# Optimization experiments

Hardware: AMD Instinct MI355X
Metric: run time of the kernel (lower is better)

## Reference

```python
import jax, jax.numpy as jnp
import numpy as np

NUM_SCOPES, NUM_DECOMPS, BATCH, NUM_IN, NUM_SUMS = 32, 8, 256, 256, 256


def setup_inputs() -> dict:
    key = jax.random.key(0)
    k1, k2 = jax.random.split(key)
    # x: log-probabilities from children, shape [scopes, decomps, batch, num_nodes_in]
    x = jax.random.normal(k1, (NUM_SCOPES, NUM_DECOMPS, BATCH, NUM_IN), dtype=jnp.float32)
    # accumulators: positive weights, shape [scopes, decomps, num_nodes_in, num_sums]
    accumulators = jax.random.uniform(
        k2, (NUM_SCOPES, NUM_DECOMPS, NUM_IN, NUM_SUMS), dtype=jnp.float32,
        minval=1e-3, maxval=1.0)
    return {"x": x, "accumulators": accumulators}


def _logmatmul(x, logw):
    # out[s,d,b,j] = logsumexp_i( x[s,d,b,i] + logw[s,d,i,j] )
    # Stable form: factor out per-row / per-col maxes, do a real GEMM in linear space.
    xmax = jnp.max(x, axis=3, keepdims=True)            # [s,d,b,1]
    wmax = jnp.max(logw, axis=2, keepdims=True)         # [s,d,1,j]
    y = jnp.einsum('sdbi,sdij->sdbj', jnp.exp(x - xmax), jnp.exp(logw - wmax))
    return jnp.log(y) + xmax + wmax                     # [s,d,b,j]


def reference(x, accumulators):
    # Default path: logspace_accumulators=False, backprop_mode=GRADIENT
    log_weights = jax.nn.log_softmax(jnp.log(accumulators), axis=2)
    return _logmatmul(x, log_weights)
```

## Files before the change

kernel.cpp:

```cpp
#include <hip/hip_runtime.h>


#define NB  256
#define NI  256
#define NJ  256
#define BH  128

typedef __attribute__((ext_vector_type(8))) short bf16x8;
typedef __attribute__((ext_vector_type(4))) float f32x4;

__device__ __forceinline__ unsigned short f2bf(float f) {
  unsigned int u = __float_as_uint(f);
  u += 0x7FFFu + ((u >> 16) & 1u);
  return (unsigned short)(u >> 16);
}

__global__ __launch_bounds__(512, 2)
void densesum_kernel(const float* __restrict__ x,
                     const float* __restrict__ acc,
                     float* __restrict__ out) {
  const int sd = blockIdx.x;
  const float* xb = x   + (size_t)sd * NB * NI;
  const float* ab = acc + (size_t)sd * NI * NJ;
  float*       ob = out + (size_t)sd * NB * NJ;

  __shared__ unsigned short As[BH * 64];
  __shared__ unsigned short Bs[NJ * NI];
  __shared__ float colpart[8 * NJ];
  __shared__ float logS[NJ];

  const int tid  = threadIdx.x;
  const int lane = tid & 63;
  const int wid  = tid >> 6;
  const int wr   = wid >> 2;
  const int wc   = wid & 3;
  const int l15  = lane & 15;
  const int lk   = lane >> 4;
  const int r    = (lane >> 1) & 3;
  const bool s1 = (r & 1), s2 = (r & 2);

  f32x4 C[4][4];
  float bsum0 = 0.f, bsum1 = 0.f, bsum2 = 0.f, bsum3 = 0.f;
  float4 pa[4];
  float4 pb[8];

  auto zeroC = [&]() {
    #pragma unroll
    for (int m = 0; m < 4; ++m)
      #pragma unroll
      for (int n = 0; n < 4; ++n)
        C[m][n] = (f32x4){0.f, 0.f, 0.f, 0.f};
  };

  auto loadA = [&](const float* xh, int kc) {
    #pragma unroll
    for (int it = 0; it < 4; ++it) {
      int q  = tid + it * 512;
      int b  = q >> 4;
      int c0 = (q & 15) * 4;
      pa[it] = *reinterpret_cast<const float4*>(xh + (size_t)b * NI + kc * 64 + c0);
    }
  };
  auto loadB = [&](int kc) {
    #pragma unroll
    for (int t = 0; t < 2; ++t) {
      int q  = tid + t * 512;
      int kl = (q >> 6) * 4;
      int jb = (q & 63) * 4;
      const float* src = ab + (size_t)(kc * 64 + kl) * NJ + jb;
      pb[t * 4 + 0] = *reinterpret_cast<const float4*>(src);
      pb[t * 4 + 1] = *reinterpret_cast<const float4*>(src + NJ);
      pb[t * 4 + 2] = *reinterpret_cast<const float4*>(src + 2 * NJ);
      pb[t * 4 + 3] = *reinterpret_cast<const float4*>(src + 3 * NJ);
    }
  };
  auto convA = [&]() {
    #pragma unroll
    for (int it = 0; it < 4; ++it) {
      int q  = tid + it * 512;
      int b  = q >> 4;
      int c0 = (q & 15) * 4;
      ushort4 h;
      h.x = f2bf(__expf(pa[it].x));
      h.y = f2bf(__expf(pa[it].y));
      h.z = f2bf(__expf(pa[it].z));
      h.w = f2bf(__expf(pa[it].w));
      *reinterpret_cast<ushort4*>(&As[b * 64 + (c0 ^ ((b & 7) << 3))]) = h;
    }
  };
  auto convB = [&](int kc) {
    #pragma unroll
    for (int t = 0; t < 2; ++t) {
      int q   = tid + t * 512;
      int kl  = (q >> 6) * 4;
      int jb  = (q & 63) * 4;
      int kg  = kc * 64 + kl;
      float4 v0 = pb[t * 4 + 0], v1 = pb[t * 4 + 1];
      float4 v2 = pb[t * 4 + 2], v3 = pb[t * 4 + 3];
      #define ROT(v, u0, u1, u2, u3)                                            \
        { float t0 = s1 ? v.y : v.x, t1 = s1 ? v.z : v.y,                       \
                t2 = s1 ? v.w : v.z, t3 = s1 ? v.x : v.w;                       \
          u0 = s2 ? t2 : t0; u1 = s2 ? t3 : t1;                                 \
          u2 = s2 ? t0 : t2; u3 = s2 ? t1 : t3; }
      float a00, a01, a02, a03; ROT(v0, a00, a01, a02, a03);
      float a10, a11, a12, a13; ROT(v1, a10, a11, a12, a13);
      float a20, a21, a22, a23; ROT(v2, a20, a21, a22, a23);
      float a30, a31, a32, a33; ROT(v3, a30, a31, a32, a33);
      #undef ROT
      #define STORE_COL(cc, w0, w1, w2, w3)                                     \
        { int jc = jb + ((cc + r) & 3);                                         \
          bsum##cc += w0 + w1 + w2 + w3;                                        \
          ushort4 h; h.x = f2bf(w0); h.y = f2bf(w1);                            \
          h.z = f2bf(w2); h.w = f2bf(w3);                                       \
          *reinterpret_cast<ushort4*>(&Bs[jc * NI + (kg ^ ((jc & 7) << 3))]) = h; }
      STORE_COL(0, a00, a10, a20, a30);
      STORE_COL(1, a01, a11, a21, a31);
      STORE_COL(2, a02, a12, a22, a32);
      STORE_COL(3, a03, a13, a23, a33);
      #undef STORE_COL
    }
  };
  auto mfmaChunk = [&](int kc) {
    #pragma unroll
    for (int ks = 0; ks < 2; ++ks) {
      const int ka = ks * 32 + 8 * lk;
      const int kg = kc * 64 + ka;
      bf16x8 bfr[4];
      #pragma unroll
      for (int n = 0; n < 4; ++n) {
        int row = wc * 64 + n * 16 + l15;
        bfr[n] = *reinterpret_cast<const bf16x8*>(&Bs[row * NI + (kg ^ ((row & 7) << 3))]);
      }
      #pragma unroll
      for (int m = 0; m < 4; ++m) {
        int row = wr * 64 + m * 16 + l15;
        bf16x8 af = *reinterpret_cast<const bf16x8*>(&As[row * 64 + (ka ^ ((row & 7) << 3))]);
        #pragma unroll
        for (int n = 0; n < 4; ++n)
          C[m][n] = __builtin_amdgcn_mfma_f32_16x16x32_bf16(af, bfr[n], C[m][n], 0, 0, 0);
      }
    }
  };
  auto epilogue = [&](int bh) {
    float* obh = ob + (size_t)bh * BH * NJ;
    #pragma unroll
    for (int m = 0; m < 4; ++m) {
      int b0 = wr * 64 + m * 16 + lk * 4;
      #pragma unroll
      for (int n = 0; n < 4; ++n) {
        int j = wc * 64 + n * 16 + l15;
        float ls = logS[j];
        #pragma unroll
        for (int rr = 0; rr < 4; ++rr) {
          obh[(size_t)(b0 + rr) * NJ + j] = __logf(C[m][n][rr]) - ls;
        }
      }
    }
  };

  loadA(xb, 0);
  loadB(0);
  zeroC();
  for (int kc = 0; kc < 4; ++kc) {
    convA();
    convB(kc);
    __syncthreads();
    if (kc < 3) {
      loadA(xb, kc + 1);
      loadB(kc + 1);
    } else {
      loadA(xb + (size_t)BH * NI, 0);
    }
    mfmaChunk(kc);
    __syncthreads();
  }

  {
    int jb = lane * 4;
    colpart[wid * NJ + jb + ((0 + r) & 3)] = bsum0;
    colpart[wid * NJ + jb + ((1 + r) & 3)] = bsum1;
    colpart[wid * NJ + jb + ((2 + r) & 3)] = bsum2;
    colpart[wid * NJ + jb + ((3 + r) & 3)] = bsum3;
  }
  __syncthreads();
  if (tid < NJ) {
    float s = 0.f;
    #pragma unroll
    for (int c = 0; c < 8; ++c) s += colpart[c * NJ + tid];
    logS[tid] = __logf(s);
  }
  __syncthreads();

  epilogue(0);

  zeroC();
  for (int kc = 0; kc < 4; ++kc) {
    convA();
    __syncthreads();
    if (kc < 3) loadA(xb + (size_t)BH * NI, kc + 1);
    mfmaChunk(kc);
    __syncthreads();
  }

  epilogue(1);
}

extern "C" void kernel_launch(void* const* d_in, const int* in_sizes, int n_in,
                              void* d_out, int out_size, void* d_ws, size_t ws_size,
                              hipStream_t stream) {
  const float* x   = (const float*)d_in[0];
  const float* acc = (const float*)d_in[1];
  float* out = (float*)d_out;
  hipLaunchKernelGGL(densesum_kernel, dim3(256), dim3(512), 0, stream, x, acc, out);
}
```

Baseline: 38.25 us.

## Double block size to 1024 threads with 16 waves splitting output columns

Launches 1024 threads per block instead of 512 and rearranges the wave grid to 2x8, so each wave computes a 64x32 output tile instead of 64x64. The load and convert work per thread for A and B is halved, and the column-sum reduction gains an extra pairwise stage through shared memory. The aim is more waves per CU to hide memory latency and exp/convert cost. In exchange the register budget per thread is tighter, each B fragment is reused over fewer columns, and the extra reduction stage adds a barrier.

```diff
diff --git a/kernel.cpp b/kernel.cpp
--- a/kernel.cpp
+++ b/kernel.cpp
@@ -15,7 +15,7 @@
   return (unsigned short)(u >> 16);
 }
 
-__global__ __launch_bounds__(512, 2)
+__global__ __launch_bounds__(1024, 4)
 void densesum_kernel(const float* __restrict__ x,
                      const float* __restrict__ acc,
                      float* __restrict__ out) {
@@ -26,58 +26,54 @@
 
   __shared__ unsigned short As[BH * 64];
   __shared__ unsigned short Bs[NJ * NI];
-  __shared__ float colpart[8 * NJ];
+  __shared__ float redbuf[8 * NJ];
   __shared__ float logS[NJ];
 
   const int tid  = threadIdx.x;
   const int lane = tid & 63;
   const int wid  = tid >> 6;
-  const int wr   = wid >> 2;
-  const int wc   = wid & 3;
+  const int wr   = wid >> 3;
+  const int wc   = wid & 7;
   const int l15  = lane & 15;
   const int lk   = lane >> 4;
   const int r    = (lane >> 1) & 3;
   const bool s1 = (r & 1), s2 = (r & 2);
-
-  f32x4 C[4][4];
+  const int kp   = wid;
+  const int jbB  = lane * 4;
+
+  f32x4 C[4][2];
   float bsum0 = 0.f, bsum1 = 0.f, bsum2 = 0.f, bsum3 = 0.f;
-  float4 pa[4];
-  float4 pb[8];
+  float4 pa[2];
+  float4 pb[4];
 
   auto zeroC = [&]() {
     #pragma unroll
     for (int m = 0; m < 4; ++m)
       #pragma unroll
-      for (int n = 0; n < 4; ++n)
+      for (int n = 0; n < 2; ++n)
         C[m][n] = (f32x4){0.f, 0.f, 0.f, 0.f};
   };
 
   auto loadA = [&](const float* xh, int kc) {
     #pragma unroll
-    for (int it = 0; it < 4; ++it) {
-      int q  = tid + it * 512;
+    for (int it = 0; it < 2; ++it) {
+      int q  = tid + it * 1024;
       int b  = q >> 4;
       int c0 = (q & 15) * 4;
       pa[it] = *reinterpret_cast<const float4*>(xh + (size_t)b * NI + kc * 64 + c0);
     }
   };
   auto loadB = [&](int kc) {
-    #pragma unroll
-    for (int t = 0; t < 2; ++t) {
-      int q  = tid + t * 512;
-      int kl = (q >> 6) * 4;
-      int jb = (q & 63) * 4;
-      const float* src = ab + (size_t)(kc * 64 + kl) * NJ + jb;
-      pb[t * 4 + 0] = *reinterpret_cast<const float4*>(src);
-      pb[t * 4 + 1] = *reinterpret_cast<const float4*>(src + NJ);
-      pb[t * 4 + 2] = *reinterpret_cast<const float4*>(src + 2 * NJ);
-      pb[t * 4 + 3] = *reinterpret_cast<const float4*>(src + 3 * NJ);
-    }
+    const float* src = ab + (size_t)(kc * 64 + kp * 4) * NJ + jbB;
+    pb[0] = *reinterpret_cast<const float4*>(src);
+    pb[1] = *reinterpret_cast<const float4*>(src + NJ);
+    pb[2] = *reinterpret_cast<const float4*>(src + 2 * NJ);
+    pb[3] = *reinterpret_cast<const float4*>(src + 3 * NJ);
   };
   auto convA = [&]() {
     #pragma unroll
-    for (int it = 0; it < 4; ++it) {
-      int q  = tid + it * 512;
+    for (int it = 0; it < 2; ++it) {
+      int q  = tid + it * 1024;
       int b  = q >> 4;
       int c0 = (q & 15) * 4;
       ushort4 h;
@@ -89,46 +85,39 @@
     }
   };
   auto convB = [&](int kc) {
-    #pragma unroll
-    for (int t = 0; t < 2; ++t) {
-      int q   = tid + t * 512;
-      int kl  = (q >> 6) * 4;
-      int jb  = (q & 63) * 4;
-      int kg  = kc * 64 + kl;
-      float4 v0 = pb[t * 4 + 0], v1 = pb[t * 4 + 1];
-      float4 v2 = pb[t * 4 + 2], v3 = pb[t * 4 + 3];
-      #define ROT(v, u0, u1, u2, u3)                                            \
-        { float t0 = s1 ? v.y : v.x, t1 = s1 ? v.z : v.y,                       \
-                t2 = s1 ? v.w : v.z, t3 = s1 ? v.x : v.w;                       \
-          u0 = s2 ? t2 : t0; u1 = s2 ? t3 : t1;                                 \
-          u2 = s2 ? t0 : t2; u3 = s2 ? t1 : t3; }
-      float a00, a01, a02, a03; ROT(v0, a00, a01, a02, a03);
-      float a10, a11, a12, a13; ROT(v1, a10, a11, a12, a13);
-      float a20, a21, a22, a23; ROT(v2, a20, a21, a22, a23);
-      float a30, a31, a32, a33; ROT(v3, a30, a31, a32, a33);
-      #undef ROT
-      #define STORE_COL(cc, w0, w1, w2, w3)                                     \
-        { int jc = jb + ((cc + r) & 3);                                         \
-          bsum##cc += w0 + w1 + w2 + w3;                                        \
-          ushort4 h; h.x = f2bf(w0); h.y = f2bf(w1);                            \
-          h.z = f2bf(w2); h.w = f2bf(w3);                                       \
-          *reinterpret_cast<ushort4*>(&Bs[jc * NI + (kg ^ ((jc & 7) << 3))]) = h; }
-      STORE_COL(0, a00, a10, a20, a30);
-      STORE_COL(1, a01, a11, a21, a31);
-      STORE_COL(2, a02, a12, a22, a32);
-      STORE_COL(3, a03, a13, a23, a33);
-      #undef STORE_COL
-    }
+    const int kg = kc * 64 + kp * 4;
+    float4 v0 = pb[0], v1 = pb[1], v2 = pb[2], v3 = pb[3];
+    #define ROT(v, u0, u1, u2, u3)                                              \
+      { float t0 = s1 ? v.y : v.x, t1 = s1 ? v.z : v.y,                         \
+              t2 = s1 ? v.w : v.z, t3 = s1 ? v.x : v.w;                         \
+        u0 = s2 ? t2 : t0; u1 = s2 ? t3 : t1;                                   \
+        u2 = s2 ? t0 : t2; u3 = s2 ? t1 : t3; }
+    float a00, a01, a02, a03; ROT(v0, a00, a01, a02, a03);
+    float a10, a11, a12, a13; ROT(v1, a10, a11, a12, a13);
+    float a20, a21, a22, a23; ROT(v2, a20, a21, a22, a23);
+    float a30, a31, a32, a33; ROT(v3, a30, a31, a32, a33);
+    #undef ROT
+    #define STORE_COL(cc, w0, w1, w2, w3)                                       \
+      { int jc = jbB + ((cc + r) & 3);                                          \
+        bsum##cc += w0 + w1 + w2 + w3;                                          \
+        ushort4 h; h.x = f2bf(w0); h.y = f2bf(w1);                              \
+        h.z = f2bf(w2); h.w = f2bf(w3);                                         \
+        *reinterpret_cast<ushort4*>(&Bs[jc * NI + (kg ^ ((jc & 7) << 3))]) = h; }
+    STORE_COL(0, a00, a10, a20, a30);
+    STORE_COL(1, a01, a11, a21, a31);
+    STORE_COL(2, a02, a12, a22, a32);
+    STORE_COL(3, a03, a13, a23, a33);
+    #undef STORE_COL
   };
   auto mfmaChunk = [&](int kc) {
     #pragma unroll
     for (int ks = 0; ks < 2; ++ks) {
       const int ka = ks * 32 + 8 * lk;
       const int kg = kc * 64 + ka;
-      bf16x8 bfr[4];
-      #pragma unroll
-      for (int n = 0; n < 4; ++n) {
-        int row = wc * 64 + n * 16 + l15;
+      bf16x8 bfr[2];
+      #pragma unroll
+      for (int n = 0; n < 2; ++n) {
+        int row = wc * 32 + n * 16 + l15;
         bfr[n] = *reinterpret_cast<const bf16x8*>(&Bs[row * NI + (kg ^ ((row & 7) << 3))]);
       }
       #pragma unroll
@@ -136,7 +125,7 @@
         int row = wr * 64 + m * 16 + l15;
         bf16x8 af = *reinterpret_cast<const bf16x8*>(&As[row * 64 + (ka ^ ((row & 7) << 3))]);
         #pragma unroll
-        for (int n = 0; n < 4; ++n)
+        for (int n = 0; n < 2; ++n)
           C[m][n] = __builtin_amdgcn_mfma_f32_16x16x32_bf16(af, bfr[n], C[m][n], 0, 0, 0);
       }
     }
@@ -147,8 +136,8 @@
     for (int m = 0; m < 4; ++m) {
       int b0 = wr * 64 + m * 16 + lk * 4;
       #pragma unroll
-      for (int n = 0; n < 4; ++n) {
-        int j = wc * 64 + n * 16 + l15;
+      for (int n = 0; n < 2; ++n) {
+        int j = wc * 32 + n * 16 + l15;
         float ls = logS[j];
         #pragma unroll
         for (int rr = 0; rr < 4; ++rr) {
@@ -175,18 +164,26 @@
     __syncthreads();
   }
 
-  {
-    int jb = lane * 4;
-    colpart[wid * NJ + jb + ((0 + r) & 3)] = bsum0;
-    colpart[wid * NJ + jb + ((1 + r) & 3)] = bsum1;
-    colpart[wid * NJ + jb + ((2 + r) & 3)] = bsum2;
-    colpart[wid * NJ + jb + ((3 + r) & 3)] = bsum3;
+  if (wid >= 8) {
+    float* row = &redbuf[(wid - 8) * NJ];
+    row[jbB + ((0 + r) & 3)] = bsum0;
+    row[jbB + ((1 + r) & 3)] = bsum1;
+    row[jbB + ((2 + r) & 3)] = bsum2;
+    row[jbB + ((3 + r) & 3)] = bsum3;
+  }
+  __syncthreads();
+  if (wid < 8) {
+    float* row = &redbuf[wid * NJ];
+    row[jbB + ((0 + r) & 3)] += bsum0;
+    row[jbB + ((1 + r) & 3)] += bsum1;
+    row[jbB + ((2 + r) & 3)] += bsum2;
+    row[jbB + ((3 + r) & 3)] += bsum3;
   }
   __syncthreads();
   if (tid < NJ) {
     float s = 0.f;
     #pragma unroll
-    for (int c = 0; c < 8; ++c) s += colpart[c * NJ + tid];
+    for (int c = 0; c < 8; ++c) s += redbuf[c * NJ + tid];
     logS[tid] = __logf(s);
   }
   __syncthreads();
@@ -211,5 +208,5 @@
   const float* x   = (const float*)d_in[0];
   const float* acc = (const float*)d_in[1];
   float* out = (float*)d_out;
-  hipLaunchKernelGGL(densesum_kernel, dim3(256), dim3(512), 0, stream, x, acc, out);
+  hipLaunchKernelGGL(densesum_kernel, dim3(256), dim3(1024), 0, stream, x, acc, out);
 }
```

Measured after the change: 39.06 us. 2.1% more time.
